# Kernel tuning notes

Measured on AMD Instinct MI355X. Metric: run time of the kernel, lower is better.

The kernel has to match this reference:

```python
import jax, jax.numpy as jnp
import numpy as np

HEADS = 8
DIM_HEAD = 64
SCALE = DIM_HEAD ** -0.5


def setup_inputs() -> dict:
    key = jax.random.key(0)
    k1, k2, k3, k4 = jax.random.split(key, 4)
    b, c, f, h, w = 2, 512, 16, 32, 32
    x = jax.random.normal(k1, (b, c, f, h, w), dtype=jnp.float32)
    pos_bias = jax.random.normal(k2, (HEADS, f, f), dtype=jnp.float32)
    # torch Linear(dim, 3*hidden, bias=False): store as (in, out) for right-matmul
    w_qkv = jax.random.normal(k3, (c, 3 * HEADS * DIM_HEAD), dtype=jnp.float32) * (c ** -0.5)
    w_out = jax.random.normal(k4, (HEADS * DIM_HEAD, c), dtype=jnp.float32) * ((HEADS * DIM_HEAD) ** -0.5)
    return {"x": x, "pos_bias": pos_bias, "w_qkv": w_qkv, "w_out": w_out}


def reference(x, pos_bias, w_qkv, w_out):
    b, c, f, h, w = x.shape
    # 'b c f h w -> (b h w) f c'
    xt = jnp.transpose(x, (0, 3, 4, 2, 1)).reshape(b * h * w, f, c)
    qkv = xt @ w_qkv  # (B, f, 3*hidden)
    q, k, v = jnp.split(qkv, 3, axis=-1)
    def to_heads(t):  # (B, f, h*d) -> (B, heads, f, d)
        return t.reshape(t.shape[0], f, HEADS, DIM_HEAD).transpose(0, 2, 1, 3)
    q, k, v = to_heads(q) * SCALE, to_heads(k), to_heads(v)
    sim = jnp.einsum('bhid,bhjd->bhij', q, k)
    sim = sim + pos_bias  # (heads, f, f) broadcasts over batch
    attn = jax.nn.softmax(sim, axis=-1)  # stable max-subtract softmax
    out = jnp.einsum('bhij,bhjd->bhid', attn, v)
    out = out.transpose(0, 2, 1, 3).reshape(b * h * w, f, HEADS * DIM_HEAD)
    out = out @ w_out  # (B, f, c)
    # '(b h w) f c -> b c f h w'
    return out.reshape(b, h, w, f, c).transpose(0, 4, 3, 1, 2)
```

## Files before the change

kernel.cpp:

```cpp
#include <hip/hip_runtime.h>

typedef unsigned short u16;
typedef unsigned int u32;
typedef unsigned long long u64;
typedef __attribute__((ext_vector_type(8))) short short8;
typedef __attribute__((ext_vector_type(4))) float f32x4;

__device__ __forceinline__ u16 f2bf(float f) {
  u32 u = __builtin_bit_cast(u32, f);
  u += 0x7fffu + ((u >> 16) & 1u);
  return (u16)(u >> 16);
}
__device__ __forceinline__ u32 pk2bf(float a, float b) {
  return (u32)f2bf(a) | ((u32)f2bf(b) << 16);
}

__device__ __forceinline__ void async16(const void* g, void* l) {
  __builtin_amdgcn_global_load_lds(
      (const __attribute__((address_space(1))) u32*)g,
      (__attribute__((address_space(3))) u32*)l, 16, 0, 0);
}

__global__ __launch_bounds__(256) void k_prep(const float* __restrict__ x,
                                              const float* __restrict__ w_qkv,
                                              const float* __restrict__ w_out,
                                              u16* __restrict__ XT,
                                              u16* __restrict__ WQ,
                                              u16* __restrict__ WO) {
  __shared__ char smem[4608];
  int bid = blockIdx.x;
  const int t = threadIdx.x;
  if (bid < 1024) {
    const float* in;
    u16* outT;
    int N, scaleN, perm;
    if (bid < 768) { in = w_qkv; outT = WQ; N = 1536; scaleN = 512; perm = 0; }
    else { bid -= 768; in = w_out; outT = WO; N = 512; scaleN = 0; perm = 1; }
    const int K = 512;
    const int ntiles = N >> 5;
    const int nt = bid % ntiles, kt = bid / ntiles;
    const int n0 = nt << 5, k0 = kt << 5;
    float (*tile)[33] = (float(*)[33])smem;
#pragma unroll
    for (int i = 0; i < 4; ++i) {
      const int e = t + i * 256, r = e >> 5, c = e & 31;
      tile[c][r] = in[(size_t)(k0 + r) * N + n0 + c];
    }
    __syncthreads();
#pragma unroll
    for (int i = 0; i < 4; ++i) {
      const int e = t + i * 256, r = e >> 5, c = e & 31;
      float v = tile[r][c];
      if (n0 + r < scaleN) v *= 0.125f;
      const int kcol = k0 + c;
      const int kp = perm ? ((kcol & ~63) | ((kcol & 15) << 2) | ((kcol >> 4) & 3))
                          : kcol;
      outT[(size_t)(n0 + r) * K + kp] = f2bf(v);
    }
  } else {
    bid -= 1024;
    const int plane = bid & 31;
    const int rest = bid >> 5;
    const int mt = rest & 31, ct = rest >> 5;
    const int bb = plane >> 4, f = plane & 15;
    const int m0 = mt << 5, c0 = ct << 5;
    float (*tile)[36] = (float(*)[36])smem;
    const int lr = t >> 3, lc = t & 7;
    const float4 v4 = *(const float4*)
        &x[((size_t)((bb * 512 + c0 + lr) * 16 + f)) * 1024 + m0 + lc * 4];
    *(float4*)&tile[lr][lc * 4] = v4;
    __syncthreads();
    const int m = t >> 3, cc = t & 7;
    union { u32 uu[2]; u64 q; } pk;
    pk.uu[0] = pk2bf(tile[cc * 4 + 0][m], tile[cc * 4 + 1][m]);
    pk.uu[1] = pk2bf(tile[cc * 4 + 2][m], tile[cc * 4 + 3][m]);
    *(u64*)&XT[((size_t)((bb * 1024 + m0 + m) * 16 + f)) * 512 + c0 + cc * 4] = pk.q;
  }
}

struct A3St32 { u16 A[128][32]; u16 B[192][32]; };
struct A3At { u16 q[8][16][64]; u16 k[8][16][64]; u16 vt[8][64][16]; u16 pad[16]; };
union A3Sm { A3St32 st[2]; A3At at; };

__global__ __launch_bounds__(256) void k_qkv_attn(const u16* __restrict__ XT,
                                                  const u16* __restrict__ WQ,
                                                  const float* __restrict__ pos_bias,
                                                  u16* __restrict__ AO) {
  const int tid = threadIdx.x;
  const int w = tid >> 6, lane = tid & 63;
  const int c15 = lane & 15, quad = lane >> 4;
  const int bid = blockIdx.x;
  const int hd = bid >> 8, m0 = (bid & 255) << 7;

  __shared__ A3Sm sm;

  const int lr16 = lane >> 2, lc4 = lane & 3;

  const u16* aptr[2];
  const u16* bptr[3];
#pragma unroll
  for (int t2 = 0; t2 < 2; ++t2) {
    const int r = w * 32 + t2 * 16 + lr16;
    aptr[t2] = XT + (size_t)(m0 + r) * 512 + ((lc4 ^ ((r >> 1) & 3)) << 3);
  }
#pragma unroll
  for (int t2 = 0; t2 < 3; ++t2) {
    const int j = w * 48 + t2 * 16 + lr16;
    const int grow = (j >> 6) * 512 + hd * 64 + (j & 63);
    bptr[t2] = WQ + (size_t)grow * 512 + ((lc4 ^ ((j >> 1) & 3)) << 3);
  }

  f32x4 acc[3][8];
#pragma unroll
  for (int c = 0; c < 3; ++c)
#pragma unroll
    for (int mt = 0; mt < 8; ++mt) acc[c][mt] = f32x4{0.f, 0.f, 0.f, 0.f};

#pragma unroll
  for (int t2 = 0; t2 < 2; ++t2)
    async16(aptr[t2], &sm.st[0].A[w * 32 + t2 * 16][0]);
#pragma unroll
  for (int t2 = 0; t2 < 3; ++t2)
    async16(bptr[t2], &sm.st[0].B[w * 48 + t2 * 16][0]);
  __syncthreads();

#pragma unroll
  for (int kk = 0; kk < 16; ++kk) {
    const int cur = kk & 1, nxt = cur ^ 1;
    if (kk < 15) {
#pragma unroll
      for (int t2 = 0; t2 < 2; ++t2)
        async16(aptr[t2] + ((kk + 1) << 5), &sm.st[nxt].A[w * 32 + t2 * 16][0]);
#pragma unroll
      for (int t2 = 0; t2 < 3; ++t2)
        async16(bptr[t2] + ((kk + 1) << 5), &sm.st[nxt].B[w * 48 + t2 * 16][0]);
    }
    short8 af[8], bt[3];
#pragma unroll
    for (int mt = 0; mt < 8; ++mt) {
      const int row = mt * 16 + c15;
      const int swz = (quad ^ ((row >> 1) & 3)) << 3;
      af[mt] = *(const short8*)&sm.st[cur].A[row][swz];
    }
#pragma unroll
    for (int c = 0; c < 3; ++c) {
      const int row = c * 64 + w * 16 + c15;
      const int swz = (quad ^ ((row >> 1) & 3)) << 3;
      bt[c] = *(const short8*)&sm.st[cur].B[row][swz];
    }
#pragma unroll
    for (int c = 0; c < 3; ++c)
#pragma unroll
      for (int mt = 0; mt < 8; ++mt)
        acc[c][mt] = __builtin_amdgcn_mfma_f32_16x16x32_bf16(af[mt], bt[c], acc[c][mt], 0, 0, 0);
    __syncthreads();
  }

  const int dloc = w * 16 + c15;
  const int ch_b = dloc >> 3, dl = dloc & 7;
#pragma unroll
  for (int mt = 0; mt < 8; ++mt) {
#pragma unroll
    for (int r = 0; r < 4; ++r) {
      const int f = quad * 4 + r;
      const int sw = ((ch_b ^ (f & 7)) << 3) | dl;
      sm.at.q[mt][f][sw] = f2bf(acc[0][mt][r]);
      sm.at.k[mt][f][sw] = f2bf(acc[1][mt][r]);
    }
    union { u32 uu[2]; u64 q; } pv;
    pv.uu[0] = pk2bf(acc[2][mt][0], acc[2][mt][1]);
    pv.uu[1] = pk2bf(acc[2][mt][2], acc[2][mt][3]);
    *(u64*)&sm.at.vt[mt][dloc][quad * 4] = pv.q;
  }
  __syncthreads();

  float pb[4];
#pragma unroll
  for (int r = 0; r < 4; ++r)
    pb[r] = pos_bias[hd * 256 + (quad * 4 + r) * 16 + c15];

  for (int sblk = 0; sblk < 2; ++sblk) {
    const int s = w * 2 + sblk;
    f32x4 sacc = f32x4{0.f, 0.f, 0.f, 0.f};
#pragma unroll
    for (int h = 0; h < 2; ++h) {
      const int chunk = (((h << 2) + quad) ^ (c15 & 7)) << 3;
      const short8 aq = *(const short8*)&sm.at.q[s][c15][chunk];
      const short8 bk = *(const short8*)&sm.at.k[s][c15][chunk];
      sacc = __builtin_amdgcn_mfma_f32_16x16x32_bf16(aq, bk, sacc, 0, 0, 0);
    }
    asm volatile("" ::: "memory");
    u16* lp = &sm.at.q[s][0][0];
#pragma unroll
    for (int e = 0; e < 4; ++e) lp[c15 * 32 + 16 + quad * 4 + e] = 0;
#pragma unroll
    for (int r = 0; r < 4; ++r) {
      float sv = sacc[r] + pb[r];
      float mx = sv;
      mx = fmaxf(mx, __shfl_xor(mx, 1));
      mx = fmaxf(mx, __shfl_xor(mx, 2));
      mx = fmaxf(mx, __shfl_xor(mx, 4));
      mx = fmaxf(mx, __shfl_xor(mx, 8));
      const float e = __expf(sv - mx);
      float sum = e;
      sum += __shfl_xor(sum, 1);
      sum += __shfl_xor(sum, 2);
      sum += __shfl_xor(sum, 4);
      sum += __shfl_xor(sum, 8);
      lp[(quad * 4 + r) * 32 + c15] = f2bf(e / sum);
    }
    asm volatile("" ::: "memory");
    const short8 ap = *(const short8*)&lp[c15 * 32 + quad * 8];
    f32x4 oacc[4];
#pragma unroll
    for (int t = 0; t < 4; ++t) {
      const short8 bv = *(const short8*)&sm.at.vt[s][t * 16 + c15][(quad & 1) * 8];
      oacc[t] = __builtin_amdgcn_mfma_f32_16x16x32_bf16(ap, bv, f32x4{0.f, 0.f, 0.f, 0.f}, 0, 0, 0);
    }
    const int s_g = (m0 >> 4) + s;
    const int bb = s_g >> 10, sp = s_g & 1023;
#pragma unroll
    for (int r = 0; r < 4; ++r) {
      union { u32 uu[2]; uint2 v; } pk;
      pk.uu[0] = pk2bf(oacc[0][r], oacc[1][r]);
      pk.uu[1] = pk2bf(oacc[2][r], oacc[3][r]);
      *(uint2*)(AO + ((size_t)(bb * 16384 + (quad * 4 + r) * 1024 + sp)) * 512 +
                hd * 64 + c15 * 4) = pk.v;
    }
  }
}

struct K2St { u16 A[128][64]; u16 B[128][64]; };

__global__ __launch_bounds__(256) void k_proj(const u16* __restrict__ AO,
                                              const u16* __restrict__ WO,
                                              float* __restrict__ out) {
  const int tid = threadIdx.x, w = tid >> 6, lane = tid & 63;
  const int c15 = lane & 15, quad = lane >> 4;
  const int bid = blockIdx.x;
  const int mb = bid & 255, nb = bid >> 8;
  const int m0 = mb << 7, n0 = nb << 7;
  const int b = m0 >> 14, mloc = m0 & 16383;
  __shared__ K2St sm;
  f32x4 acc[8][2];
#pragma unroll
  for (int mt = 0; mt < 8; ++mt) {
    acc[mt][0] = f32x4{0.f, 0.f, 0.f, 0.f};
    acc[mt][1] = f32x4{0.f, 0.f, 0.f, 0.f};
  }
  const int lr = lane >> 3, lcb = lane & 7;
  const u16* aptr[4];
  const u16* bptr[4];
#pragma unroll
  for (int t2 = 0; t2 < 4; ++t2) {
    const int r = w * 32 + t2 * 8 + lr;
    const int sw = (lcb ^ (r & 7)) << 3;
    aptr[t2] = AO + (size_t)(m0 + r) * 512 + sw;
    bptr[t2] = WO + (size_t)(n0 + r) * 512 + sw;
  }
#pragma unroll
  for (int kk = 0; kk < 8; ++kk) {
    __syncthreads();
#pragma unroll
    for (int t2 = 0; t2 < 4; ++t2) {
      async16(aptr[t2] + (kk << 6), &sm.A[w * 32 + t2 * 8][0]);
      async16(bptr[t2] + (kk << 6), &sm.B[w * 32 + t2 * 8][0]);
    }
    __syncthreads();
#pragma unroll
    for (int half = 0; half < 2; ++half) {
      short8 af[8], bt[2];
#pragma unroll
      for (int mt = 0; mt < 8; ++mt) {
        const int row = mt * 16 + c15;
        const int swz = (((half << 2) + quad) ^ (row & 7)) << 3;
        af[mt] = *(const short8*)&sm.A[row][swz];
      }
#pragma unroll
      for (int nt = 0; nt < 2; ++nt) {
        const int row = w * 32 + nt * 16 + c15;
        const int swz = (((half << 2) + quad) ^ (row & 7)) << 3;
        bt[nt] = *(const short8*)&sm.B[row][swz];
      }
#pragma unroll
      for (int mt = 0; mt < 8; ++mt) {
        acc[mt][0] = __builtin_amdgcn_mfma_f32_16x16x32_bf16(af[mt], bt[0], acc[mt][0], 0, 0, 0);
        acc[mt][1] = __builtin_amdgcn_mfma_f32_16x16x32_bf16(af[mt], bt[1], acc[mt][1], 0, 0, 0);
      }
    }
  }
  float* const obase = out + (size_t)b * 512 * 16384 + mloc + quad * 4;
#pragma unroll
  for (int nt = 0; nt < 2; ++nt) {
    const int ch = n0 + w * 32 + nt * 16 + c15;
    float* const orow = obase + (size_t)ch * 16384;
#pragma unroll
    for (int mt = 0; mt < 8; ++mt)
      *(f32x4*)&orow[mt * 16] = acc[mt][nt];
  }
}

extern "C" void kernel_launch(void* const* d_in, const int* in_sizes, int n_in,
                              void* d_out, int out_size, void* d_ws, size_t ws_size,
                              hipStream_t stream) {
  const float* x = (const float*)d_in[0];
  const float* pos_bias = (const float*)d_in[1];
  const float* w_qkv = (const float*)d_in[2];
  const float* w_out = (const float*)d_in[3];
  float* out = (float*)d_out;
  char* ws = (char*)d_ws;
  u16* XT = (u16*)(ws);
  u16* AO = (u16*)(ws + (size_t)33554432);
  u16* WQ = (u16*)(ws + (size_t)67108864);
  u16* WO = (u16*)(ws + (size_t)68681728);

  hipLaunchKernelGGL(k_prep, dim3(17408), dim3(256), 0, stream, x, w_qkv, w_out, XT, WQ, WO);
  hipLaunchKernelGGL(k_qkv_attn, dim3(2048), dim3(256), 0, stream, XT, WQ, pos_bias, AO);
  hipLaunchKernelGGL(k_proj, dim3(1024), dim3(256), 0, stream, AO, WO, out);
}
```

Before: 228.0 us.

## Compute V per-wave for its own sequences and pass it via shuffles, not LDS

The V projection is repartitioned so each wave computes V only for the two 16-frame sequences it later attends over, keeping V in registers and delivering the B operand of the PV MFMA through cross-lane shuffles instead of an LDS transpose buffer. This drops the vt array from shared memory, shrinking the attention-phase LDS footprint. A launch-bounds hint of four blocks per SM is added to push occupancy. The cost is extra LDS reads of A and V-weight rows per k-step and shuffle instructions, plus possible register pressure or spills under the tighter launch bound.

```diff
diff --git a/kernel.cpp b/kernel.cpp
--- a/kernel.cpp
+++ b/kernel.cpp
@@ -79,13 +79,13 @@
 }
 
 struct A3St32 { u16 A[128][32]; u16 B[192][32]; };
-struct A3At { u16 q[8][16][64]; u16 k[8][16][64]; u16 vt[8][64][16]; u16 pad[16]; };
+struct A3At { u16 q[8][16][64]; u16 k[8][16][64]; };
 union A3Sm { A3St32 st[2]; A3At at; };
 
-__global__ __launch_bounds__(256) void k_qkv_attn(const u16* __restrict__ XT,
-                                                  const u16* __restrict__ WQ,
-                                                  const float* __restrict__ pos_bias,
-                                                  u16* __restrict__ AO) {
+__global__ __launch_bounds__(256, 4) void k_qkv_attn(const u16* __restrict__ XT,
+                                                     const u16* __restrict__ WQ,
+                                                     const float* __restrict__ pos_bias,
+                                                     u16* __restrict__ AO) {
   const int tid = threadIdx.x;
   const int w = tid >> 6, lane = tid & 63;
   const int c15 = lane & 15, quad = lane >> 4;
@@ -110,11 +110,16 @@
     bptr[t2] = WQ + (size_t)grow * 512 + ((lc4 ^ ((j >> 1) & 3)) << 3);
   }
 
-  f32x4 acc[3][8];
-#pragma unroll
-  for (int c = 0; c < 3; ++c)
+  f32x4 acc[2][8];
+  f32x4 accv[2][4];
+#pragma unroll
+  for (int c = 0; c < 2; ++c)
 #pragma unroll
     for (int mt = 0; mt < 8; ++mt) acc[c][mt] = f32x4{0.f, 0.f, 0.f, 0.f};
+#pragma unroll
+  for (int si = 0; si < 2; ++si)
+#pragma unroll
+    for (int nt = 0; nt < 4; ++nt) accv[si][nt] = f32x4{0.f, 0.f, 0.f, 0.f};
 
 #pragma unroll
   for (int t2 = 0; t2 < 2; ++t2)
@@ -135,7 +140,7 @@
       for (int t2 = 0; t2 < 3; ++t2)
         async16(bptr[t2] + ((kk + 1) << 5), &sm.st[nxt].B[w * 48 + t2 * 16][0]);
     }
-    short8 af[8], bt[3];
+    short8 af[8], bt[2], btv[4], av[2];
 #pragma unroll
     for (int mt = 0; mt < 8; ++mt) {
       const int row = mt * 16 + c15;
@@ -143,16 +148,33 @@
       af[mt] = *(const short8*)&sm.st[cur].A[row][swz];
     }
 #pragma unroll
-    for (int c = 0; c < 3; ++c) {
+    for (int c = 0; c < 2; ++c) {
       const int row = c * 64 + w * 16 + c15;
       const int swz = (quad ^ ((row >> 1) & 3)) << 3;
       bt[c] = *(const short8*)&sm.st[cur].B[row][swz];
     }
 #pragma unroll
-    for (int c = 0; c < 3; ++c)
+    for (int nt = 0; nt < 4; ++nt) {
+      const int row = 128 + nt * 16 + c15;
+      const int swz = (quad ^ ((row >> 1) & 3)) << 3;
+      btv[nt] = *(const short8*)&sm.st[cur].B[row][swz];
+    }
+#pragma unroll
+    for (int si = 0; si < 2; ++si) {
+      const int row = w * 32 + si * 16 + c15;
+      const int swz = (quad ^ ((row >> 1) & 3)) << 3;
+      av[si] = *(const short8*)&sm.st[cur].A[row][swz];
+    }
+#pragma unroll
+    for (int c = 0; c < 2; ++c)
 #pragma unroll
       for (int mt = 0; mt < 8; ++mt)
         acc[c][mt] = __builtin_amdgcn_mfma_f32_16x16x32_bf16(af[mt], bt[c], acc[c][mt], 0, 0, 0);
+#pragma unroll
+    for (int si = 0; si < 2; ++si)
+#pragma unroll
+      for (int nt = 0; nt < 4; ++nt)
+        accv[si][nt] = __builtin_amdgcn_mfma_f32_16x16x32_bf16(av[si], btv[nt], accv[si][nt], 0, 0, 0);
     __syncthreads();
   }
 
@@ -167,11 +189,15 @@
       sm.at.q[mt][f][sw] = f2bf(acc[0][mt][r]);
       sm.at.k[mt][f][sw] = f2bf(acc[1][mt][r]);
     }
-    union { u32 uu[2]; u64 q; } pv;
-    pv.uu[0] = pk2bf(acc[2][mt][0], acc[2][mt][1]);
-    pv.uu[1] = pk2bf(acc[2][mt][2], acc[2][mt][3]);
-    *(u64*)&sm.at.vt[mt][dloc][quad * 4] = pv.q;
-  }
+  }
+  u32 pv01[2][4], pv23[2][4];
+#pragma unroll
+  for (int si = 0; si < 2; ++si)
+#pragma unroll
+    for (int nt = 0; nt < 4; ++nt) {
+      pv01[si][nt] = pk2bf(accv[si][nt][0], accv[si][nt][1]);
+      pv23[si][nt] = pk2bf(accv[si][nt][2], accv[si][nt][3]);
+    }
   __syncthreads();
 
   float pb[4];
@@ -179,6 +205,7 @@
   for (int r = 0; r < 4; ++r)
     pb[r] = pos_bias[hd * 256 + (quad * 4 + r) * 16 + c15];
 
+#pragma unroll
   for (int sblk = 0; sblk < 2; ++sblk) {
     const int s = w * 2 + sblk;
     f32x4 sacc = f32x4{0.f, 0.f, 0.f, 0.f};
@@ -211,11 +238,16 @@
     }
     asm volatile("" ::: "memory");
     const short8 ap = *(const short8*)&lp[c15 * 32 + quad * 8];
+    const int vsrc = c15 + ((quad & 1) << 5);
     f32x4 oacc[4];
 #pragma unroll
     for (int t = 0; t < 4; ++t) {
-      const short8 bv = *(const short8*)&sm.at.vt[s][t * 16 + c15][(quad & 1) * 8];
-      oacc[t] = __builtin_amdgcn_mfma_f32_16x16x32_bf16(ap, bv, f32x4{0.f, 0.f, 0.f, 0.f}, 0, 0, 0);
+      union { u32 uu[4]; short8 s8; } bvv;
+      bvv.uu[0] = __shfl(pv01[sblk][t], vsrc);
+      bvv.uu[1] = __shfl(pv23[sblk][t], vsrc);
+      bvv.uu[2] = __shfl(pv01[sblk][t], vsrc + 16);
+      bvv.uu[3] = __shfl(pv23[sblk][t], vsrc + 16);
+      oacc[t] = __builtin_amdgcn_mfma_f32_16x16x32_bf16(ap, bvv.s8, f32x4{0.f, 0.f, 0.f, 0.f}, 0, 0, 0);
     }
     const int s_g = (m0 >> 4) + s;
     const int bb = s_g >> 10, sp = s_g & 1023;
```

Measured after the change: 673.6 us. 195% more time.
